# Optimization experiments

Hardware: AMD Instinct MI355X
Metric: run time of the kernel (lower is better)

Reference implementation:

```python
import jax, jax.numpy as jnp
import numpy as np

NEG_INF = -1e9
LEAKY_SLOPE = 0.2


def setup_inputs() -> dict:
    key = jax.random.key(0)
    k1, k2, k3, k4, k5, k6, k7 = jax.random.split(key, 7)
    B, L = 50000, 50          # batch nodes, max padded neighbors (num_sample)
    N = 200000                # unique node embeddings
    D_in, D_out = 256, 64
    padded_neighs = jax.random.randint(k1, (B, L), 0, N, dtype=jnp.int32)
    mask = jax.random.randint(k2, (B, L), 0, 2, dtype=jnp.int32).astype(jnp.bool_)
    mask = mask.at[:, 0].set(True)  # every node has >=1 neighbor
    dst_idx = jax.random.randint(k3, (B,), 0, N, dtype=jnp.int32)
    embed_table = jax.random.normal(k4, (N, D_in), dtype=jnp.float32)
    # xavier_uniform for proj [D_out, D_in]
    bound = float(np.sqrt(6.0 / (D_in + D_out)))
    W_proj = jax.random.uniform(k5, (D_out, D_in), minval=-bound, maxval=bound, dtype=jnp.float32)
    a_src = jax.random.normal(k6, (D_out,), dtype=jnp.float32) * 0.1
    a_dst = jax.random.normal(k7, (D_out,), dtype=jnp.float32) * 0.1
    return {"padded_neighs": padded_neighs, "mask": mask, "dst_idx": dst_idx,
            "embed_table": embed_table, "W_proj": W_proj, "a_src": a_src, "a_dst": a_dst}


def leaky_relu(x):
    return jnp.where(x >= 0, x, LEAKY_SLOPE * x)


def reference(padded_neighs, mask, dst_idx, embed_table, W_proj, a_src, a_dst):
    # project all unique-node embeddings: [N, D_out]
    embed_prime = embed_table @ W_proj.T
    # gather neighbor and dst projected features
    neigh_feats = embed_prime[padded_neighs]          # [B, L, D_out]
    dst_feats = embed_prime[dst_idx]                  # [B, D_out] (constant across L)
    # GAT-style scores: leaky_relu(dst @ a_dst) + leaky_relu(neigh @ a_src)
    dst_attn = leaky_relu(dst_feats @ a_dst)[:, None, None]       # [B, 1, 1]
    neigh_attn = leaky_relu(neigh_feats @ a_src)[:, :, None]      # [B, L, 1]
    edge_attn = dst_attn + neigh_attn                             # [B, L, 1]
    # masked softmax over the neighbor axis
    scores = jnp.where(mask[:, :, None], edge_attn, NEG_INF)
    attn = jax.nn.softmax(scores, axis=1)                         # [B, L, 1]
    # weighted sum of neighbor features
    return jnp.sum(attn * neigh_feats, axis=1)                    # [B, D_out]
```

## Files before the change

### kernel.cpp

```cpp
#include <hip/hip_runtime.h>
#include <stdint.h>

#define DIN 256
#define DOUT 64
#define LMAX 50
#define NEG_INF -1e9f
#define WSTRIDE 264

typedef short bf16x8 __attribute__((ext_vector_type(8)));
typedef float f32x4  __attribute__((ext_vector_type(4)));

static __device__ __forceinline__ unsigned short f2bf(float x) {
    unsigned int u = __float_as_uint(x);
    u += 0x7fffu + ((u >> 16) & 1u);
    return (unsigned short)(u >> 16);
}
static __device__ __forceinline__ float bflo(unsigned int u) { return __uint_as_float(u << 16); }
static __device__ __forceinline__ float bfhi(unsigned int u) { return __uint_as_float(u & 0xffff0000u); }

__global__ __launch_bounds__(256) void proj_kernel(
    const float* __restrict__ embed, const float* __restrict__ W,
    unsigned short* __restrict__ ep16, int N)
{
    __shared__ unsigned short wl[64 * WSTRIDE];

    const int tid  = threadIdx.x;
    const int lane = tid & 63;
    const int wv   = tid >> 6;
    const int mrow = lane & 15;
    const int quad = lane >> 4;

#pragma unroll
    for (int i = 0; i < 16; ++i) {
        const int idx4 = tid + 256 * i;
        const int e    = idx4 * 4;
        const int n    = e >> 8;
        const int k    = e & 255;
        const float4 f = *(const float4*)&W[e];
        union { unsigned short s[4]; unsigned long long v; } p;
        p.s[0] = f2bf(f.x); p.s[1] = f2bf(f.y);
        p.s[2] = f2bf(f.z); p.s[3] = f2bf(f.w);
        *(unsigned long long*)&wl[n * WSTRIDE + k] = p.v;
    }
    __syncthreads();

    const int m_base = blockIdx.x * 128 + wv * 32;

    f32x4 acc[2][4];
#pragma unroll
    for (int mt = 0; mt < 2; ++mt)
#pragma unroll
        for (int nt = 0; nt < 4; ++nt) acc[mt][nt] = (f32x4){0.f, 0.f, 0.f, 0.f};

    for (int kc = 0; kc < DIN; kc += 32) {
        bf16x8 afrag[2];
#pragma unroll
        for (int mt = 0; mt < 2; ++mt) {
            int row = m_base + mt * 16 + mrow;
            if (row >= N) row = N - 1;
            const float* ap = embed + (size_t)row * DIN + kc + quad * 8;
            const float4 f0 = *(const float4*)ap;
            const float4 f1 = *(const float4*)(ap + 4);
            union { short s[8]; bf16x8 f; } a;
            a.s[0] = (short)f2bf(f0.x); a.s[1] = (short)f2bf(f0.y);
            a.s[2] = (short)f2bf(f0.z); a.s[3] = (short)f2bf(f0.w);
            a.s[4] = (short)f2bf(f1.x); a.s[5] = (short)f2bf(f1.y);
            a.s[6] = (short)f2bf(f1.z); a.s[7] = (short)f2bf(f1.w);
            afrag[mt] = a.f;
        }
#pragma unroll
        for (int nt = 0; nt < 4; ++nt) {
            const bf16x8 bfrag =
                *(const bf16x8*)&wl[(nt * 16 + mrow) * WSTRIDE + kc + quad * 8];
            acc[0][nt] = __builtin_amdgcn_mfma_f32_16x16x32_bf16(
                afrag[0], bfrag, acc[0][nt], 0, 0, 0);
            acc[1][nt] = __builtin_amdgcn_mfma_f32_16x16x32_bf16(
                afrag[1], bfrag, acc[1][nt], 0, 0, 0);
        }
    }

#pragma unroll
    for (int mt = 0; mt < 2; ++mt)
#pragma unroll
        for (int nt = 0; nt < 4; ++nt)
#pragma unroll
            for (int r = 0; r < 4; ++r) {
                const int row = m_base + mt * 16 + quad * 4 + r;
                if (row < N)
                    ep16[(size_t)row * DOUT + nt * 16 + mrow] = f2bf(acc[mt][nt][r]);
            }
}

__global__ __launch_bounds__(256, 6) void agg_kernel(
    const int* __restrict__ neighs, const void* __restrict__ mask,
    const unsigned int* __restrict__ ep16u,
    const float* __restrict__ a_src,
    float* __restrict__ out, int B)
{
    __shared__ unsigned int fwbuf[4][LMAX * 32];

    const int tid  = threadIdx.x;
    const int lane = tid & 63;
    const int wv   = tid >> 6;
    const int b    = blockIdx.x * 4 + wv;
    const int bc   = b < B ? b : B - 1;

    const unsigned int* mw = (const unsigned int*)mask;
    const bool byteMode = (mw[12] > 1u);

    const int* nb = neighs + (size_t)bc * LMAX;
    bool mvalid = false;
    int  nbv    = 0;
    if (lane < LMAX) {
        const int mi = bc * LMAX + lane;
        mvalid = byteMode ? (((const uint8_t*)mask)[mi] != 0)
                          : (((const int*)mask)[mi] != 0);
        nbv = nb[lane];
    }
    const unsigned long long vm = __ballot(mvalid);
    const int nv = (int)__popcll(vm);

    const int p    = (int)__popcll(vm & ((1ull << lane) - 1ull));
    const int dsta = mvalid ? p : (nv + (lane - p));
    const int cnb  = __builtin_amdgcn_ds_permute(dsta << 2, nbv);

    unsigned int* buf = fwbuf[wv];
    const int sub    = lane >> 3;
    const int gchunk = (lane & 7) ^ sub;
    const int f      = nv >> 3;
    for (int i = 0; i < f; ++i) {
        const int r = 8 * i + sub;
        const int n = __shfl(cnb, r, 64);
        const unsigned int* gp = ep16u + (size_t)n * 32 + gchunk * 4;
        __builtin_amdgcn_global_load_lds(
            (const __attribute__((address_space(1))) void*)gp,
            (__attribute__((address_space(3))) void*)&buf[i * 256],
            16, 0, 0);
    }
    const int t     = nv & 7;
    const int npair = (t + 1) >> 1;
    const int rbase = 8 * f;
    for (int p2 = 0; p2 < npair; ++p2) {
        const int r   = rbase + 2 * p2 + (lane >> 5);
        const int rc  = r < nv ? r : nv - 1;
        const int n   = __shfl(cnb, rc, 64);
        const int w   = lane & 31;
        const int gwd = (((w >> 2) ^ (r & 7)) << 2) + (w & 3);
        const unsigned int* gp = ep16u + (size_t)n * 32 + gwd;
        __builtin_amdgcn_global_load_lds(
            (const __attribute__((address_space(1))) void*)gp,
            (__attribute__((address_space(3))) void*)&buf[(rbase + 2 * p2) * 32],
            4, 0, 0);
    }

    asm volatile("s_waitcnt vmcnt(0)" ::: "memory");

    const int lc   = lane < nv ? lane : nv - 1;
    const int rot7 = lc & 7;
    const unsigned int* fr = buf + lc * 32;
    float dot = 0.f;
#pragma unroll
    for (int k8 = 0; k8 < 8; ++k8) {
        const uint4 u = *(const uint4*)&fr[((k8 ^ rot7) << 2)];
        dot = fmaf(bflo(u.x), a_src[k8 * 8 + 0], dot);
        dot = fmaf(bfhi(u.x), a_src[k8 * 8 + 1], dot);
        dot = fmaf(bflo(u.y), a_src[k8 * 8 + 2], dot);
        dot = fmaf(bfhi(u.y), a_src[k8 * 8 + 3], dot);
        dot = fmaf(bflo(u.z), a_src[k8 * 8 + 4], dot);
        dot = fmaf(bfhi(u.z), a_src[k8 * 8 + 5], dot);
        dot = fmaf(bflo(u.w), a_src[k8 * 8 + 6], dot);
        dot = fmaf(bfhi(u.w), a_src[k8 * 8 + 7], dot);
    }
    const float lr = dot >= 0.f ? dot : 0.2f * dot;
    float s = (lane < nv) ? lr : NEG_INF;

    float mx = s;
#pragma unroll
    for (int m = 32; m >= 1; m >>= 1) mx = fmaxf(mx, __shfl_xor(mx, m, 64));
    const float e = __expf(s - mx);
    float se = e;
#pragma unroll
    for (int m = 32; m >= 1; m >>= 1) se += __shfl_xor(se, m, 64);
    const float attn = e / se;

    const int s8   = lane >> 3;
    const int gc   = lane & 7;
    const int nit8 = (nv + 7) >> 3;

    float acc[8];
#pragma unroll
    for (int j = 0; j < 8; ++j) acc[j] = 0.f;

    int  rr0 = s8 < nv ? s8 : nv - 1;
    uint4 u  = *(const uint4*)&buf[rr0 * 32 + ((gc ^ (rr0 & 7)) << 2)];
    float w  = __shfl(attn, s8, 64);

    for (int i = 0; i < nit8; ++i) {
        const int inx = (i + 1 < nit8) ? i + 1 : i;
        const int r   = 8 * inx + s8;
        const int rr  = r < nv ? r : nv - 1;
        const uint4 un = *(const uint4*)&buf[rr * 32 + ((gc ^ (rr & 7)) << 2)];
        const float wn = __shfl(attn, r, 64);
        acc[0] = fmaf(w, bflo(u.x), acc[0]);
        acc[1] = fmaf(w, bfhi(u.x), acc[1]);
        acc[2] = fmaf(w, bflo(u.y), acc[2]);
        acc[3] = fmaf(w, bfhi(u.y), acc[3]);
        acc[4] = fmaf(w, bflo(u.z), acc[4]);
        acc[5] = fmaf(w, bfhi(u.z), acc[5]);
        acc[6] = fmaf(w, bflo(u.w), acc[6]);
        acc[7] = fmaf(w, bfhi(u.w), acc[7]);
        u = un; w = wn;
    }

#pragma unroll
    for (int m = 8; m <= 32; m <<= 1)
#pragma unroll
        for (int j = 0; j < 8; ++j) acc[j] += __shfl_xor(acc[j], m, 64);

    if (b < B && lane < 8) {
        float* op = out + (size_t)b * DOUT + 8 * lane;
        float4 o0; o0.x = acc[0]; o0.y = acc[1]; o0.z = acc[2]; o0.w = acc[3];
        float4 o1; o1.x = acc[4]; o1.y = acc[5]; o1.z = acc[6]; o1.w = acc[7];
        *(float4*)op       = o0;
        *(float4*)(op + 4) = o1;
    }
}

extern "C" void kernel_launch(void* const* d_in, const int* in_sizes, int n_in,
                              void* d_out, int out_size, void* d_ws, size_t ws_size,
                              hipStream_t stream)
{
    const int*   neighs  = (const int*)d_in[0];
    const void*  mask    = d_in[1];
    const float* embed   = (const float*)d_in[3];
    const float* W       = (const float*)d_in[4];
    const float* a_src   = (const float*)d_in[5];
    float* out = (float*)d_out;

    const int B = in_sizes[2];
    const int N = in_sizes[3] / DIN;

    unsigned short* ep16 = (unsigned short*)d_ws;

    proj_kernel<<<dim3((N + 127) / 128), dim3(256), 0, stream>>>(embed, W, ep16, N);
    agg_kernel<<<dim3((B + 3) / 4), dim3(256), 0, stream>>>(
        neighs, mask, (const unsigned int*)ep16, a_src, out, B);
}
```

Baseline: 357.5 us.

## Stage embedding tile in LDS with coalesced loads in projection kernel

The projection kernel now loads a 64-row embedding tile with fully coalesced float4 loads, converts it to bf16 into shared memory, and feeds MFMA A-fragments from LDS instead of strided per-lane global loads. Each block now covers 64 rows (16 per wave) instead of 128, doubling the grid. This targets uncoalesced global access on the 200 MB embedding read, at the cost of doubled LDS use (about 67 KB per block), which limits occupancy, and no overlap between loading and compute.

```diff
diff --git a/kernel.cpp b/kernel.cpp
--- a/kernel.cpp
+++ b/kernel.cpp
@@ -23,12 +23,14 @@
     unsigned short* __restrict__ ep16, int N)
 {
     __shared__ unsigned short wl[64 * WSTRIDE];
+    __shared__ unsigned short al[64 * WSTRIDE];
 
     const int tid  = threadIdx.x;
     const int lane = tid & 63;
     const int wv   = tid >> 6;
     const int mrow = lane & 15;
     const int quad = lane >> 4;
+    const int m_base = blockIdx.x * 64;
 
 #pragma unroll
     for (int i = 0; i < 16; ++i) {
@@ -42,53 +44,47 @@
         p.s[2] = f2bf(f.z); p.s[3] = f2bf(f.w);
         *(unsigned long long*)&wl[n * WSTRIDE + k] = p.v;
     }
+#pragma unroll
+    for (int i = 0; i < 16; ++i) {
+        const int idx4 = tid + 256 * i;
+        const int e    = idx4 * 4;
+        const int n    = e >> 8;
+        const int k    = e & 255;
+        int row = m_base + n;
+        if (row >= N) row = N - 1;
+        const float4 f = *(const float4*)&embed[(size_t)row * DIN + k];
+        union { unsigned short s[4]; unsigned long long v; } p;
+        p.s[0] = f2bf(f.x); p.s[1] = f2bf(f.y);
+        p.s[2] = f2bf(f.z); p.s[3] = f2bf(f.w);
+        *(unsigned long long*)&al[n * WSTRIDE + k] = p.v;
+    }
     __syncthreads();
 
-    const int m_base = blockIdx.x * 128 + wv * 32;
-
-    f32x4 acc[2][4];
-#pragma unroll
-    for (int mt = 0; mt < 2; ++mt)
-#pragma unroll
-        for (int nt = 0; nt < 4; ++nt) acc[mt][nt] = (f32x4){0.f, 0.f, 0.f, 0.f};
-
+    f32x4 acc[4];
+#pragma unroll
+    for (int nt = 0; nt < 4; ++nt) acc[nt] = (f32x4){0.f, 0.f, 0.f, 0.f};
+
+#pragma unroll
     for (int kc = 0; kc < DIN; kc += 32) {
-        bf16x8 afrag[2];
-#pragma unroll
-        for (int mt = 0; mt < 2; ++mt) {
-            int row = m_base + mt * 16 + mrow;
-            if (row >= N) row = N - 1;
-            const float* ap = embed + (size_t)row * DIN + kc + quad * 8;
-            const float4 f0 = *(const float4*)ap;
-            const float4 f1 = *(const float4*)(ap + 4);
-            union { short s[8]; bf16x8 f; } a;
-            a.s[0] = (short)f2bf(f0.x); a.s[1] = (short)f2bf(f0.y);
-            a.s[2] = (short)f2bf(f0.z); a.s[3] = (short)f2bf(f0.w);
-            a.s[4] = (short)f2bf(f1.x); a.s[5] = (short)f2bf(f1.y);
-            a.s[6] = (short)f2bf(f1.z); a.s[7] = (short)f2bf(f1.w);
-            afrag[mt] = a.f;
-        }
+        const bf16x8 afrag =
+            *(const bf16x8*)&al[(wv * 16 + mrow) * WSTRIDE + kc + quad * 8];
 #pragma unroll
         for (int nt = 0; nt < 4; ++nt) {
             const bf16x8 bfrag =
                 *(const bf16x8*)&wl[(nt * 16 + mrow) * WSTRIDE + kc + quad * 8];
-            acc[0][nt] = __builtin_amdgcn_mfma_f32_16x16x32_bf16(
-                afrag[0], bfrag, acc[0][nt], 0, 0, 0);
-            acc[1][nt] = __builtin_amdgcn_mfma_f32_16x16x32_bf16(
-                afrag[1], bfrag, acc[1][nt], 0, 0, 0);
+            acc[nt] = __builtin_amdgcn_mfma_f32_16x16x32_bf16(
+                afrag, bfrag, acc[nt], 0, 0, 0);
         }
     }
 
 #pragma unroll
-    for (int mt = 0; mt < 2; ++mt)
-#pragma unroll
-        for (int nt = 0; nt < 4; ++nt)
-#pragma unroll
-            for (int r = 0; r < 4; ++r) {
-                const int row = m_base + mt * 16 + quad * 4 + r;
-                if (row < N)
-                    ep16[(size_t)row * DOUT + nt * 16 + mrow] = f2bf(acc[mt][nt][r]);
-            }
+    for (int nt = 0; nt < 4; ++nt)
+#pragma unroll
+        for (int r = 0; r < 4; ++r) {
+            const int row = m_base + wv * 16 + quad * 4 + r;
+            if (row < N)
+                ep16[(size_t)row * DOUT + nt * 16 + mrow] = f2bf(acc[nt][r]);
+        }
 }
 
 __global__ __launch_bounds__(256, 6) void agg_kernel(
@@ -242,7 +238,7 @@
 
     unsigned short* ep16 = (unsigned short*)d_ws;
 
-    proj_kernel<<<dim3((N + 127) / 128), dim3(256), 0, stream>>>(embed, W, ep16, N);
+    proj_kernel<<<dim3((N + 63) / 64), dim3(256), 0, stream>>>(embed, W, ep16, N);
     agg_kernel<<<dim3((B + 3) / 4), dim3(256), 0, stream>>>(
         neighs, mask, (const unsigned int*)ep16, a_src, out, B);
 }
```

New measurement: 349.2 us. 1.02x faster.
